# Kernel optimization log

Hardware: AMD Instinct MI355X
Metric: run time of the kernel (lower is better)

## Reference

```python
import jax, jax.numpy as jnp
import numpy as np

CH = 256
B, H, W = 8, 64, 64


def _conv1x1(x, w, b):
    # x: [b, cin, h, w], w: [cout, cin], b: [cout]
    return jnp.einsum('bchw,oc->bohw', x, w) + b[None, :, None, None]


def setup_inputs() -> dict:
    key = jax.random.key(0)
    ks = jax.random.split(key, 6)
    s = 0.05  # weight scale (spectral-norm keeps weights O(1); scaled for stable softmax)
    return {
        'x': jax.random.normal(ks[0], (B, CH, H, W), dtype=jnp.float32),
        'wf': jax.random.normal(ks[1], (CH // 8, CH), dtype=jnp.float32) * s,
        'bf': jnp.zeros((CH // 8,), dtype=jnp.float32),
        'wg': jax.random.normal(ks[2], (CH // 8, CH), dtype=jnp.float32) * s,
        'bg': jnp.zeros((CH // 8,), dtype=jnp.float32),
        'wh': jax.random.normal(ks[3], (CH // 2, CH), dtype=jnp.float32) * s,
        'bh': jnp.zeros((CH // 2,), dtype=jnp.float32),
        'wv': jax.random.normal(ks[4], (CH, CH // 2), dtype=jnp.float32) * s,
        'bv': jnp.zeros((CH,), dtype=jnp.float32),
        'gamma': jnp.ones((1,), dtype=jnp.float32) * 0.5,
    }


def reference(x, wf, bf, wg, bg, wh, bh, wv, bv, gamma):
    b, c, h, w = x.shape
    n = h * w
    f = _conv1x1(x, wf, bf).reshape(b, -1, n)   # [b, c/8, n]
    g = _conv1x1(x, wg, bg).reshape(b, -1, n)   # [b, c/8, n]
    # scores = f^T g : [b, n, n]; softmax over last dim
    beta = jax.nn.softmax(jnp.einsum('bkn,bkm->bnm', f, g), axis=-1)
    h_ = _conv1x1(x, wh, bh).reshape(b, -1, n)  # [b, c/2, n]
    o = jnp.einsum('bcn,bnm->bcm', h_, beta).reshape(b, c // 2, h, w)
    o = _conv1x1(o, wv, bv)                      # [b, c, h, w]
    return x + gamma[0] * o
```

## Files before the change

kernel.cpp:

```cpp
#include <hip/hip_runtime.h>
#include <cstdint>

typedef float f32x4 __attribute__((ext_vector_type(4)));
typedef short bf16x8 __attribute__((ext_vector_type(8)));
typedef unsigned short u16x4 __attribute__((ext_vector_type(4)));
typedef unsigned uint4v __attribute__((ext_vector_type(4)));
typedef unsigned uint2v __attribute__((ext_vector_type(2)));

#define LOG2E 1.44269504088896340736f

#if __has_builtin(__builtin_amdgcn_exp2f)
#define EXP2(v) __builtin_amdgcn_exp2f(v)
#else
#define EXP2(v) exp2f(v)
#endif
#if __has_builtin(__builtin_amdgcn_logf)
#define LOG2F(v) __builtin_amdgcn_logf(v)
#else
#define LOG2F(v) __log2f(v)
#endif

#define GLD16(gp, lp) __builtin_amdgcn_global_load_lds( \
    (const __attribute__((address_space(1))) unsigned*)(const void*)(gp), \
    (__attribute__((address_space(3))) unsigned*)(void*)(lp), 16, 0, 0)

enum : unsigned {
    WALL_OFF  = 0u,
    BALL_OFF  = 98304u,
    WVF_OFF   = 99072u,
    FF_OFF    = 164608u,
    GF_OFF    = 2261760u,
    HF_OFF    = 4358912u,
    SCALE_OFF = 12747520u,
    ZPART_OFF = 12878592u,
    PART_OFF  = 13402880u,
};

static __device__ __forceinline__ unsigned short f2bf(float f) {
    unsigned u = __builtin_bit_cast(unsigned, f);
    u += 0x7fffu + ((u >> 16) & 1u);
    return (unsigned short)(u >> 16);
}

static __device__ __forceinline__ unsigned pk_bf(float lo, float hi) {
    unsigned a = __builtin_bit_cast(unsigned, hi) + 0x8000u;
    unsigned b = __builtin_bit_cast(unsigned, lo) + 0x8000u;
    return __builtin_amdgcn_perm(a, b, 0x07060302u);
}

static __device__ __forceinline__ f32x4 mfma_bf16(bf16x8 a, bf16x8 b, f32x4 c) {
    return __builtin_amdgcn_mfma_f32_16x16x32_bf16(a, b, c, 0, 0, 0);
}

__global__ __launch_bounds__(256) void k0_pack(const float* __restrict__ wf,
                                               const float* __restrict__ bfv,
                                               const float* __restrict__ wg,
                                               const float* __restrict__ bg,
                                               const float* __restrict__ wh,
                                               const float* __restrict__ bh,
                                               const float* __restrict__ wv,
                                               unsigned char* __restrict__ ws) {
    unsigned idx = blockIdx.x * 256u + threadIdx.x;
    unsigned short* Wall = (unsigned short*)(ws + WALL_OFF);
    float* ball = (float*)(ws + BALL_OFF);
    unsigned short* wvf = (unsigned short*)(ws + WVF_OFF);
    if (idx < 49152u) {
        unsigned k = idx >> 8;
        float v;
        if (k < 32u)      v = wf[idx] * LOG2E;
        else if (k < 64u) v = wg[idx - 8192u];
        else              v = wh[idx - 16384u];
        Wall[idx] = f2bf(v);
    } else if (idx < 49344u) {
        unsigned k = idx - 49152u;
        float v;
        if (k < 32u)      v = bfv[k] * LOG2E;
        else if (k < 64u) v = bg[k - 32u];
        else              v = bh[k - 64u];
        ball[k] = v;
    } else if (idx < 82112u) {
        unsigned jj = idx - 49344u;
        unsigned cc = jj >> 7, c = jj & 127u;
        unsigned cct = cc >> 4, lv = cc & 15u;
        unsigned ksv = c >> 5, qv = (c >> 3) & 3u, jv = c & 7u;
        wvf[(((cct * 4u + ksv) * 4u + qv) * 16u + lv) * 8u + jv] = f2bf(wv[jj]);
    }
}

__global__ __launch_bounds__(256) void k1_proj(const float* __restrict__ x,
                                               unsigned char* __restrict__ ws) {
    __shared__ unsigned XT[64 * 132];
    const int b = blockIdx.y;
    const int n0 = blockIdx.x * 64;
    const unsigned short* Wall = (const unsigned short*)(ws + WALL_OFF);
    const float* ball = (const float*)(ws + BALL_OFF);
    unsigned short* Ff = (unsigned short*)(ws + FF_OFF) + b * 131072;
    unsigned short* Gf = (unsigned short*)(ws + GF_OFF) + b * 131072;
    unsigned short* Hf = (unsigned short*)(ws + HF_OFF) + b * 524288;
    const int tid = threadIdx.x;
    const float* xb = x + b * (256 * 4096) + n0;
    {
        const int n4 = (tid & 15) * 4;
        const int crow = (tid >> 4) * 2;
        #pragma unroll
        for (int it = 0; it < 8; ++it) {
            const int c = crow + it * 32;
            const f32x4 r0 = *(const f32x4*)&xb[(size_t)c * 4096 + n4];
            const f32x4 r1 = *(const f32x4*)&xb[(size_t)(c + 1) * 4096 + n4];
            #pragma unroll
            for (int j = 0; j < 4; ++j)
                XT[(n4 + j) * 132 + (c >> 1)] = pk_bf(r0[j], r1[j]);
        }
    }
    __syncthreads();
    const int l = tid & 15, q = (tid >> 4) & 3, w = tid >> 6;
    const int nloc = w * 16 + l;
    const int ncol = n0 + nloc;
    bf16x8 bX[8];
    #pragma unroll
    for (int ks = 0; ks < 8; ++ks)
        bX[ks] = *(const bf16x8*)&XT[nloc * 132 + ks * 16 + q * 4];
    #pragma unroll
    for (int kt = 0; kt < 12; ++kt) {
        f32x4 acc = {0.f, 0.f, 0.f, 0.f};
        #pragma unroll
        for (int ks = 0; ks < 8; ++ks) {
            bf16x8 aW = *(const bf16x8*)&Wall[(kt * 16 + l) * 256 + ks * 32 + q * 8];
            acc = mfma_bf16(aW, bX[ks], acc);
        }
        const int kr0 = kt * 16 + q * 4;
        #pragma unroll
        for (int r = 0; r < 4; ++r) acc[r] += ball[kr0 + r];
        if (kt < 4) {
            const int kk = kt & 1;
            unsigned short* dst = (kt < 2) ? Ff : Gf;
            const int nt = ncol >> 4;
            const int qf = kk * 2 + (q >> 1), j0 = (q & 1) * 4;
            u16x4 pk;
            #pragma unroll
            for (int r = 0; r < 4; ++r) pk[r] = f2bf(acc[r]);
            *(u16x4*)&dst[(nt * 64 + qf * 16 + l) * 8 + j0] = pk;
        } else {
            const int ct = kt - 4;
            const int nt = ncol >> 5, qh = (ncol >> 3) & 3, jh = ncol & 7;
            #pragma unroll
            for (int r = 0; r < 4; ++r)
                Hf[((nt * 8 + ct) * 64 + qh * 16 + (q * 4 + r)) * 8 + jh] = f2bf(acc[r]);
        }
    }
}

__global__ __launch_bounds__(256) void k2_stats(unsigned char* __restrict__ ws) {
    const int b = blockIdx.y, zsl = blockIdx.z, tid = threadIdx.x;
    const int lane = tid & 63, l = tid & 15, q = (tid >> 4) & 3, w = tid >> 6;
    const unsigned short* Ff = (const unsigned short*)(ws + FF_OFF) + b * 131072;
    const unsigned short* Gf = (const unsigned short*)(ws + GF_OFF) + b * 131072;
    float* Zp = (float*)(ws + ZPART_OFF) + zsl * 32768 + b * 4096;
    const int n0 = blockIdx.x * 256 + w * 64;
    const int nt0 = n0 >> 4;
    bf16x8 aF[4];
    #pragma unroll
    for (int t = 0; t < 4; ++t)
        aF[t] = *(const bf16x8*)&Ff[((nt0 + t) * 64 + lane) * 8];
    f32x4 z[4];
    #pragma unroll
    for (int t = 0; t < 4; ++t) z[t] = (f32x4){0.f, 0.f, 0.f, 0.f};
    const int mt0 = zsl * 64;
    bf16x8 bG = *(const bf16x8*)&Gf[(mt0 * 64 + lane) * 8];
    for (int mt = 0; mt < 64; ++mt) {
        const bf16x8 g = bG;
        if (mt + 1 < 64)
            bG = *(const bf16x8*)&Gf[((mt0 + mt + 1) * 64 + lane) * 8];
        #pragma unroll
        for (int t = 0; t < 4; ++t) {
            f32x4 s = mfma_bf16(aF[t], g, (f32x4){0.f, 0.f, 0.f, 0.f});
            #pragma unroll
            for (int r = 0; r < 4; ++r)
                z[t][r] += EXP2(s[r]);
        }
    }
    #pragma unroll
    for (int off = 1; off < 16; off <<= 1)
        #pragma unroll
        for (int t = 0; t < 4; ++t)
            #pragma unroll
            for (int r = 0; r < 4; ++r)
                z[t][r] += __shfl_xor(z[t][r], off, 64);
    if (l == 0) {
        #pragma unroll
        for (int t = 0; t < 4; ++t)
            #pragma unroll
            for (int r = 0; r < 4; ++r)
                Zp[n0 + t * 16 + q * 4 + r] = z[t][r];
    }
}

__global__ __launch_bounds__(256) void k2b_inv(unsigned char* __restrict__ ws) {
    const float* zp = (const float*)(ws + ZPART_OFF);
    float* scale = (float*)(ws + SCALE_OFF);
    const int idx = (blockIdx.x * 256 + threadIdx.x) * 4;
    f32x4 s = *(const f32x4*)&zp[idx];
    s += *(const f32x4*)&zp[32768 + idx];
    s += *(const f32x4*)&zp[65536 + idx];
    s += *(const f32x4*)&zp[98304 + idx];
    f32x4 o;
    #pragma unroll
    for (int r = 0; r < 4; ++r) o[r] = -LOG2F(s[r]);
    *(f32x4*)&scale[idx] = o;
}

template<int NS>
__global__ __launch_bounds__(256, NS) void k3_attn(unsigned char* __restrict__ ws) {
    constexpr int NITER = 128 / NS;
    constexpr int NGRP = 8 * NS;
    constexpr int NQ = 4096 / NS;
    __shared__ __align__(16) unsigned short HT[2][4096];
    __shared__ __align__(16) unsigned short FTs[2][1024];
    __shared__ __align__(16) float SC[NQ];
    const int tid = threadIdx.x;
    const int lane = tid & 63, l = tid & 15, q = (tid >> 4) & 3, w = tid >> 6;
    const int g = blockIdx.x % NGRP, bxm = blockIdx.x / NGRP;
    const int b = g / NS, nh = g % NS;
    const unsigned short* Ff = (const unsigned short*)(ws + FF_OFF) + b * 131072;
    const unsigned short* Gf = (const unsigned short*)(ws + GF_OFF) + b * 131072;
    const unsigned short* Hf = (const unsigned short*)(ws + HF_OFF) + b * 524288;
    const float* lsc = (const float*)(ws + SCALE_OFF) + b * 4096 + nh * NQ;
    const int mt0 = bxm * 8 + w * 2;
    const bf16x8 bG0 = *(const bf16x8*)&Gf[(mt0 * 64 + lane) * 8];
    const bf16x8 bG1 = *(const bf16x8*)&Gf[((mt0 + 1) * 64 + lane) * 8];
    f32x4 acc0[8], acc1[8];
    #pragma unroll
    for (int ct = 0; ct < 8; ++ct) {
        acc0[ct] = (f32x4){0.f, 0.f, 0.f, 0.f};
        acc1[ct] = (f32x4){0.f, 0.f, 0.f, 0.f};
    }
    const bool qlo = q < 2;
    const int srcA = (q & 1) * 32 + l;
    const int srcB = srcA + 16;

    auto stage = [&](int i, int p) {
        const unsigned short* Hg = Hf + (size_t)(nh * NITER + i) * 4096;
        GLD16(Hg + ((w * 2 + 0) * 64 + lane) * 8, &HT[p][(w * 2 + 0) * 512]);
        GLD16(Hg + ((w * 2 + 1) * 64 + lane) * 8, &HT[p][(w * 2 + 1) * 512]);
        if (w < 2)
            GLD16(Ff + ((size_t)((nh * NITER + i) * 2 + w) * 64 + lane) * 8,
                  &FTs[p][w * 512]);
    };

    {
        constexpr int CH = NQ / 256;
        #pragma unroll
        for (int j = w; j < CH; j += 4)
            GLD16(lsc + j * 256 + lane * 4, &SC[j * 256]);
    }
    stage(0, 0);

    for (int i = 0; i < NITER; ++i) {
        const int p = i & 1;
        __syncthreads();
        if (i + 1 < NITER) stage(i + 1, p ^ 1);
        const bf16x8 aF0 = *(const bf16x8*)&FTs[p][lane * 8];
        const bf16x8 aF1 = *(const bf16x8*)&FTs[p][512 + lane * 8];
        const f32x4 c0 = *(const f32x4*)&SC[i * 32 + q * 4];
        const f32x4 c1 = *(const f32x4*)&SC[i * 32 + 16 + q * 4];
        f32x4 s0 = mfma_bf16(aF0, bG0, c0);
        f32x4 s1 = mfma_bf16(aF1, bG0, c1);
        f32x4 s2 = mfma_bf16(aF0, bG1, c0);
        f32x4 s3 = mfma_bf16(aF1, bG1, c1);
        f32x4 e0, e1, e2, e3;
        #pragma unroll
        for (int r = 0; r < 4; ++r) {
            e0[r] = EXP2(s0[r]);
            e1[r] = EXP2(s1[r]);
            e2[r] = EXP2(s2[r]);
            e3[r] = EXP2(s3[r]);
        }
        const unsigned a01 = pk_bf(e0[0], e0[1]), a23 = pk_bf(e0[2], e0[3]);
        const unsigned b01 = pk_bf(e1[0], e1[1]), b23 = pk_bf(e1[2], e1[3]);
        const unsigned g01 = pk_bf(e2[0], e2[1]), g23 = pk_bf(e2[2], e2[3]);
        const unsigned h01 = pk_bf(e3[0], e3[1]), h23 = pk_bf(e3[2], e3[3]);
        uint4v r0, r1;
        {
            int tA, tB;
            tA = __shfl((int)a01, srcA, 64); tB = __shfl((int)b01, srcA, 64);
            r0[0] = (unsigned)(qlo ? tA : tB);
            tA = __shfl((int)a23, srcA, 64); tB = __shfl((int)b23, srcA, 64);
            r0[1] = (unsigned)(qlo ? tA : tB);
            tA = __shfl((int)a01, srcB, 64); tB = __shfl((int)b01, srcB, 64);
            r0[2] = (unsigned)(qlo ? tA : tB);
            tA = __shfl((int)a23, srcB, 64); tB = __shfl((int)b23, srcB, 64);
            r0[3] = (unsigned)(qlo ? tA : tB);
            tA = __shfl((int)g01, srcA, 64); tB = __shfl((int)h01, srcA, 64);
            r1[0] = (unsigned)(qlo ? tA : tB);
            tA = __shfl((int)g23, srcA, 64); tB = __shfl((int)h23, srcA, 64);
            r1[1] = (unsigned)(qlo ? tA : tB);
            tA = __shfl((int)g01, srcB, 64); tB = __shfl((int)h01, srcB, 64);
            r1[2] = (unsigned)(qlo ? tA : tB);
            tA = __shfl((int)g23, srcB, 64); tB = __shfl((int)h23, srcB, 64);
            r1[3] = (unsigned)(qlo ? tA : tB);
        }
        const bf16x8 bE0 = __builtin_bit_cast(bf16x8, r0);
        const bf16x8 bE1 = __builtin_bit_cast(bf16x8, r1);
        #pragma unroll
        for (int ct = 0; ct < 8; ++ct) {
            const bf16x8 aH = *(const bf16x8*)&HT[p][ct * 512 + lane * 8];
            acc0[ct] = mfma_bf16(aH, bE0, acc0[ct]);
            acc1[ct] = mfma_bf16(aH, bE1, acc1[ct]);
        }
    }
    unsigned short* P = (unsigned short*)(ws + PART_OFF);
    const size_t mb = (size_t)(b * NS + nh) * 4096 + bxm * 128;
    #pragma unroll
    for (int ct = 0; ct < 8; ++ct) {
        uint2v p0, p1;
        p0[0] = pk_bf(acc0[ct][0], acc0[ct][1]);
        p0[1] = pk_bf(acc0[ct][2], acc0[ct][3]);
        p1[0] = pk_bf(acc1[ct][0], acc1[ct][1]);
        p1[1] = pk_bf(acc1[ct][2], acc1[ct][3]);
        *(uint2v*)&P[(mb + w * 32 + l) * 128 + ct * 16 + q * 4] = p0;
        *(uint2v*)&P[(mb + w * 32 + 16 + l) * 128 + ct * 16 + q * 4] = p1;
    }
}

template<int NS>
__global__ __launch_bounds__(256) void k4_out(const float* __restrict__ x,
                                              const float* __restrict__ bv,
                                              const float* __restrict__ gamma,
                                              float* __restrict__ out,
                                              unsigned char* __restrict__ ws) {
    const int b = blockIdx.y, tid = threadIdx.x;
    const int lane = tid & 63, l = tid & 15, q = (tid >> 4) & 3, w = tid >> 6;
    const unsigned short* P = (const unsigned short*)(ws + PART_OFF);
    const unsigned short* Wvf = (const unsigned short*)(ws + WVF_OFF);
    const int mg = blockIdx.x * 64 + w * 16 + l;
    bf16x8 bO[4];
    #pragma unroll
    for (int ks = 0; ks < 4; ++ks) {
        float lo[4] = {0.f, 0.f, 0.f, 0.f}, hi[4] = {0.f, 0.f, 0.f, 0.f};
        #pragma unroll
        for (int h = 0; h < NS; ++h) {
            const size_t bh = ((size_t)(b * NS + h) * 4096 + mg) * 128;
            const uint4v u = *(const uint4v*)&P[bh + ks * 32 + q * 8];
            #pragma unroll
            for (int j = 0; j < 4; ++j) {
                lo[j] += __builtin_bit_cast(float, u[j] << 16);
                hi[j] += __builtin_bit_cast(float, u[j] & 0xffff0000u);
            }
        }
        uint4v s;
        #pragma unroll
        for (int j = 0; j < 4; ++j) s[j] = pk_bf(lo[j], hi[j]);
        bO[ks] = __builtin_bit_cast(bf16x8, s);
    }
    const float gam = gamma[0];
    const float* xb = x + b * (256 * 4096);
    float* ob = out + b * (256 * 4096);
    #pragma unroll
    for (int cct = 0; cct < 16; ++cct) {
        f32x4 f = {0.f, 0.f, 0.f, 0.f};
        #pragma unroll
        for (int ks = 0; ks < 4; ++ks) {
            const bf16x8 aV = *(const bf16x8*)&Wvf[((cct * 4 + ks) * 64 + lane) * 8];
            f = mfma_bf16(aV, bO[ks], f);
        }
        #pragma unroll
        for (int r = 0; r < 4; ++r) {
            const int cc = cct * 16 + q * 4 + r;
            ob[cc * 4096 + mg] = xb[cc * 4096 + mg] + gam * (f[r] + bv[cc]);
        }
    }
}

extern "C" void kernel_launch(void* const* d_in, const int* in_sizes, int n_in,
                              void* d_out, int out_size, void* d_ws, size_t ws_size,
                              hipStream_t stream) {
    const float* x   = (const float*)d_in[0];
    const float* wf  = (const float*)d_in[1];
    const float* bfv = (const float*)d_in[2];
    const float* wg  = (const float*)d_in[3];
    const float* bg  = (const float*)d_in[4];
    const float* wh  = (const float*)d_in[5];
    const float* bh  = (const float*)d_in[6];
    const float* wv  = (const float*)d_in[7];
    const float* bv  = (const float*)d_in[8];
    const float* gam = (const float*)d_in[9];
    float* out = (float*)d_out;
    unsigned char* ws = (unsigned char*)d_ws;
    (void)in_sizes; (void)n_in; (void)out_size;

    hipLaunchKernelGGL(k0_pack, dim3(321), dim3(256), 0, stream,
                       wf, bfv, wg, bg, wh, bh, wv, ws);
    hipLaunchKernelGGL(k1_proj, dim3(64, 8), dim3(256), 0, stream, x, ws);
    hipLaunchKernelGGL(k2_stats, dim3(16, 8, 4), dim3(256), 0, stream, ws);
    hipLaunchKernelGGL(k2b_inv, dim3(32), dim3(256), 0, stream, ws);

    const size_t need4 = (size_t)PART_OFF + (size_t)8 * 4 * 4096 * 128 * 2;
    if (ws_size >= need4) {
        hipLaunchKernelGGL(HIP_KERNEL_NAME(k3_attn<4>), dim3(1024), dim3(256),
                           0, stream, ws);
        hipLaunchKernelGGL(HIP_KERNEL_NAME(k4_out<4>), dim3(64, 8), dim3(256),
                           0, stream, x, bv, gam, out, ws);
    } else {
        hipLaunchKernelGGL(HIP_KERNEL_NAME(k3_attn<2>), dim3(512), dim3(256),
                           0, stream, ws);
        hipLaunchKernelGGL(HIP_KERNEL_NAME(k4_out<2>), dim3(64, 8), dim3(256),
                           0, stream, x, bv, gam, out, ws);
    }
}
```

Before: 219.1 us.

## Fuse softmax-normalizer and output projection into attention kernel via last-block counter

Removes the separate inverse-normalizer kernel by computing -log2 of the summed partial Z directly into shared memory at the start of the attention kernel. Also removes the separate output kernel: each attention block increments an atomic counter per (batch, m-tile), and the last of the NS split blocks reduces the partials and applies the Wv projection plus residual. This saves two launches and their tail gaps, but serializes the final reduction onto the last-arriving blocks. It also relies on the counters being zeroed in the pack kernel on every call.

Result: slower. 422.4 us (+92.8%).

```diff
diff --git a/kernel.cpp b/kernel.cpp
--- a/kernel.cpp
+++ b/kernel.cpp
@@ -31,9 +31,9 @@
     FF_OFF    = 164608u,
     GF_OFF    = 2261760u,
     HF_OFF    = 4358912u,
-    SCALE_OFF = 12747520u,
     ZPART_OFF = 12878592u,
-    PART_OFF  = 13402880u,
+    CTR_OFF   = 13402880u,
+    PART_OFF  = 13404928u,
 };
 
 static __device__ __forceinline__ unsigned short f2bf(float f) {
@@ -84,6 +84,8 @@
         unsigned cct = cc >> 4, lv = cc & 15u;
         unsigned ksv = c >> 5, qv = (c >> 3) & 3u, jv = c & 7u;
         wvf[(((cct * 4u + ksv) * 4u + qv) * 16u + lv) * 8u + jv] = f2bf(wv[jj]);
+    } else if (idx < 82624u) {
+        ((int*)(ws + CTR_OFF))[idx - 82112u] = 0;
     }
 }
 
@@ -195,28 +197,19 @@
     }
 }
 
-__global__ __launch_bounds__(256) void k2b_inv(unsigned char* __restrict__ ws) {
-    const float* zp = (const float*)(ws + ZPART_OFF);
-    float* scale = (float*)(ws + SCALE_OFF);
-    const int idx = (blockIdx.x * 256 + threadIdx.x) * 4;
-    f32x4 s = *(const f32x4*)&zp[idx];
-    s += *(const f32x4*)&zp[32768 + idx];
-    s += *(const f32x4*)&zp[65536 + idx];
-    s += *(const f32x4*)&zp[98304 + idx];
-    f32x4 o;
-    #pragma unroll
-    for (int r = 0; r < 4; ++r) o[r] = -LOG2F(s[r]);
-    *(f32x4*)&scale[idx] = o;
-}
-
 template<int NS>
-__global__ __launch_bounds__(256, NS) void k3_attn(unsigned char* __restrict__ ws) {
+__global__ __launch_bounds__(256, 4) void k3_attn(const float* __restrict__ x,
+                                                  const float* __restrict__ bv,
+                                                  const float* __restrict__ gamma,
+                                                  float* __restrict__ out,
+                                                  unsigned char* __restrict__ ws) {
     constexpr int NITER = 128 / NS;
     constexpr int NGRP = 8 * NS;
     constexpr int NQ = 4096 / NS;
     __shared__ __align__(16) unsigned short HT[2][4096];
     __shared__ __align__(16) unsigned short FTs[2][1024];
     __shared__ __align__(16) float SC[NQ];
+    __shared__ int lastFlag;
     const int tid = threadIdx.x;
     const int lane = tid & 63, l = tid & 15, q = (tid >> 4) & 3, w = tid >> 6;
     const int g = blockIdx.x % NGRP, bxm = blockIdx.x / NGRP;
@@ -224,7 +217,6 @@
     const unsigned short* Ff = (const unsigned short*)(ws + FF_OFF) + b * 131072;
     const unsigned short* Gf = (const unsigned short*)(ws + GF_OFF) + b * 131072;
     const unsigned short* Hf = (const unsigned short*)(ws + HF_OFF) + b * 524288;
-    const float* lsc = (const float*)(ws + SCALE_OFF) + b * 4096 + nh * NQ;
     const int mt0 = bxm * 8 + w * 2;
     const bf16x8 bG0 = *(const bf16x8*)&Gf[(mt0 * 64 + lane) * 8];
     const bf16x8 bG1 = *(const bf16x8*)&Gf[((mt0 + 1) * 64 + lane) * 8];
@@ -247,13 +239,15 @@
                   &FTs[p][w * 512]);
     };
 
+    stage(0, 0);
     {
-        constexpr int CH = NQ / 256;
-        #pragma unroll
-        for (int j = w; j < CH; j += 4)
-            GLD16(lsc + j * 256 + lane * 4, &SC[j * 256]);
-    }
-    stage(0, 0);
+        const float* zp = (const float*)(ws + ZPART_OFF) + b * 4096 + nh * NQ;
+        #pragma unroll
+        for (int j = tid; j < NQ; j += 256) {
+            const float s = zp[j] + zp[32768 + j] + zp[65536 + j] + zp[98304 + j];
+            SC[j] = -LOG2F(s);
+        }
+    }
 
     for (int i = 0; i < NITER; ++i) {
         const int p = i & 1;
@@ -320,53 +314,56 @@
         *(uint2v*)&P[(mb + w * 32 + l) * 128 + ct * 16 + q * 4] = p0;
         *(uint2v*)&P[(mb + w * 32 + 16 + l) * 128 + ct * 16 + q * 4] = p1;
     }
-}
-
-template<int NS>
-__global__ __launch_bounds__(256) void k4_out(const float* __restrict__ x,
-                                              const float* __restrict__ bv,
-                                              const float* __restrict__ gamma,
-                                              float* __restrict__ out,
-                                              unsigned char* __restrict__ ws) {
-    const int b = blockIdx.y, tid = threadIdx.x;
-    const int lane = tid & 63, l = tid & 15, q = (tid >> 4) & 3, w = tid >> 6;
-    const unsigned short* P = (const unsigned short*)(ws + PART_OFF);
+    __syncthreads();
+    if (tid == 0) {
+        __threadfence();
+        int* ctr = (int*)(ws + CTR_OFF);
+        const int old = atomicAdd(&ctr[b * 32 + bxm], 1);
+        lastFlag = (old == NS - 1) ? 1 : 0;
+    }
+    __syncthreads();
+    if (!lastFlag) return;
+    __threadfence();
+    const unsigned short* Pr = (const unsigned short*)(ws + PART_OFF);
     const unsigned short* Wvf = (const unsigned short*)(ws + WVF_OFF);
-    const int mg = blockIdx.x * 64 + w * 16 + l;
-    bf16x8 bO[4];
-    #pragma unroll
-    for (int ks = 0; ks < 4; ++ks) {
-        float lo[4] = {0.f, 0.f, 0.f, 0.f}, hi[4] = {0.f, 0.f, 0.f, 0.f};
-        #pragma unroll
-        for (int h = 0; h < NS; ++h) {
-            const size_t bh = ((size_t)(b * NS + h) * 4096 + mg) * 128;
-            const uint4v u = *(const uint4v*)&P[bh + ks * 32 + q * 8];
-            #pragma unroll
-            for (int j = 0; j < 4; ++j) {
-                lo[j] += __builtin_bit_cast(float, u[j] << 16);
-                hi[j] += __builtin_bit_cast(float, u[j] & 0xffff0000u);
-            }
-        }
-        uint4v s;
-        #pragma unroll
-        for (int j = 0; j < 4; ++j) s[j] = pk_bf(lo[j], hi[j]);
-        bO[ks] = __builtin_bit_cast(bf16x8, s);
-    }
     const float gam = gamma[0];
     const float* xb = x + b * (256 * 4096);
     float* ob = out + b * (256 * 4096);
     #pragma unroll
-    for (int cct = 0; cct < 16; ++cct) {
-        f32x4 f = {0.f, 0.f, 0.f, 0.f};
+    for (int msub = 0; msub < 2; ++msub) {
+        const int mg = bxm * 128 + msub * 64 + w * 16 + l;
+        bf16x8 bO[4];
         #pragma unroll
         for (int ks = 0; ks < 4; ++ks) {
-            const bf16x8 aV = *(const bf16x8*)&Wvf[((cct * 4 + ks) * 64 + lane) * 8];
-            f = mfma_bf16(aV, bO[ks], f);
-        }
-        #pragma unroll
-        for (int r = 0; r < 4; ++r) {
-            const int cc = cct * 16 + q * 4 + r;
-            ob[cc * 4096 + mg] = xb[cc * 4096 + mg] + gam * (f[r] + bv[cc]);
+            float lo[4] = {0.f, 0.f, 0.f, 0.f}, hi[4] = {0.f, 0.f, 0.f, 0.f};
+            #pragma unroll
+            for (int h = 0; h < NS; ++h) {
+                const size_t bh = ((size_t)(b * NS + h) * 4096 + mg) * 128;
+                const uint4v u = *(const uint4v*)&Pr[bh + ks * 32 + q * 8];
+                #pragma unroll
+                for (int j = 0; j < 4; ++j) {
+                    lo[j] += __builtin_bit_cast(float, u[j] << 16);
+                    hi[j] += __builtin_bit_cast(float, u[j] & 0xffff0000u);
+                }
+            }
+            uint4v s;
+            #pragma unroll
+            for (int j = 0; j < 4; ++j) s[j] = pk_bf(lo[j], hi[j]);
+            bO[ks] = __builtin_bit_cast(bf16x8, s);
+        }
+        #pragma unroll
+        for (int cct = 0; cct < 16; ++cct) {
+            f32x4 f = {0.f, 0.f, 0.f, 0.f};
+            #pragma unroll
+            for (int ks = 0; ks < 4; ++ks) {
+                const bf16x8 aV = *(const bf16x8*)&Wvf[((cct * 4 + ks) * 64 + lane) * 8];
+                f = mfma_bf16(aV, bO[ks], f);
+            }
+            #pragma unroll
+            for (int r = 0; r < 4; ++r) {
+                const int cc = cct * 16 + q * 4 + r;
+                ob[cc * 4096 + mg] = xb[cc * 4096 + mg] + gam * (f[r] + bv[cc]);
+            }
         }
     }
 }
@@ -388,22 +385,17 @@
     unsigned char* ws = (unsigned char*)d_ws;
     (void)in_sizes; (void)n_in; (void)out_size;
 
-    hipLaunchKernelGGL(k0_pack, dim3(321), dim3(256), 0, stream,
+    hipLaunchKernelGGL(k0_pack, dim3(322), dim3(256), 0, stream,
                        wf, bfv, wg, bg, wh, bh, wv, ws);
     hipLaunchKernelGGL(k1_proj, dim3(64, 8), dim3(256), 0, stream, x, ws);
     hipLaunchKernelGGL(k2_stats, dim3(16, 8, 4), dim3(256), 0, stream, ws);
-    hipLaunchKernelGGL(k2b_inv, dim3(32), dim3(256), 0, stream, ws);
 
     const size_t need4 = (size_t)PART_OFF + (size_t)8 * 4 * 4096 * 128 * 2;
     if (ws_size >= need4) {
         hipLaunchKernelGGL(HIP_KERNEL_NAME(k3_attn<4>), dim3(1024), dim3(256),
-                           0, stream, ws);
-        hipLaunchKernelGGL(HIP_KERNEL_NAME(k4_out<4>), dim3(64, 8), dim3(256),
                            0, stream, x, bv, gam, out, ws);
     } else {
         hipLaunchKernelGGL(HIP_KERNEL_NAME(k3_attn<2>), dim3(512), dim3(256),
-                           0, stream, ws);
-        hipLaunchKernelGGL(HIP_KERNEL_NAME(k4_out<2>), dim3(64, 8), dim3(256),
                            0, stream, x, bv, gam, out, ws);
     }
 }
```

## Fuse softmax-normalizer kernel into attention and add eight-way key split

Applied to the files above, without the earlier changes.

Removes the separate k2b_inv launch and computes the per-query log-sum normalizer directly inside k3_attn from the four partial Z sums. It also adds an NS=8 split of the key dimension (2048 blocks) when the workspace is large enough, and fixes launch bounds at 4 waves per SIMD. This saves one kernel launch and a global round trip for the scale, and raises parallelism in the attention stage. In exchange, the k4 reduction must combine more partials and the normalizer work is repeated in every block.

After: 247.9 us. 13.2% more time.

```diff
diff --git a/kernel.cpp b/kernel.cpp
--- a/kernel.cpp
+++ b/kernel.cpp
@@ -31,9 +31,8 @@
     FF_OFF    = 164608u,
     GF_OFF    = 2261760u,
     HF_OFF    = 4358912u,
-    SCALE_OFF = 12747520u,
     ZPART_OFF = 12878592u,
-    PART_OFF  = 13402880u,
+    PART_OFF  = 13404928u,
 };
 
 static __device__ __forceinline__ unsigned short f2bf(float f) {
@@ -195,22 +194,8 @@
     }
 }
 
-__global__ __launch_bounds__(256) void k2b_inv(unsigned char* __restrict__ ws) {
-    const float* zp = (const float*)(ws + ZPART_OFF);
-    float* scale = (float*)(ws + SCALE_OFF);
-    const int idx = (blockIdx.x * 256 + threadIdx.x) * 4;
-    f32x4 s = *(const f32x4*)&zp[idx];
-    s += *(const f32x4*)&zp[32768 + idx];
-    s += *(const f32x4*)&zp[65536 + idx];
-    s += *(const f32x4*)&zp[98304 + idx];
-    f32x4 o;
-    #pragma unroll
-    for (int r = 0; r < 4; ++r) o[r] = -LOG2F(s[r]);
-    *(f32x4*)&scale[idx] = o;
-}
-
 template<int NS>
-__global__ __launch_bounds__(256, NS) void k3_attn(unsigned char* __restrict__ ws) {
+__global__ __launch_bounds__(256, 4) void k3_attn(unsigned char* __restrict__ ws) {
     constexpr int NITER = 128 / NS;
     constexpr int NGRP = 8 * NS;
     constexpr int NQ = 4096 / NS;
@@ -224,7 +209,6 @@
     const unsigned short* Ff = (const unsigned short*)(ws + FF_OFF) + b * 131072;
     const unsigned short* Gf = (const unsigned short*)(ws + GF_OFF) + b * 131072;
     const unsigned short* Hf = (const unsigned short*)(ws + HF_OFF) + b * 524288;
-    const float* lsc = (const float*)(ws + SCALE_OFF) + b * 4096 + nh * NQ;
     const int mt0 = bxm * 8 + w * 2;
     const bf16x8 bG0 = *(const bf16x8*)&Gf[(mt0 * 64 + lane) * 8];
     const bf16x8 bG1 = *(const bf16x8*)&Gf[((mt0 + 1) * 64 + lane) * 8];
@@ -247,13 +231,15 @@
                   &FTs[p][w * 512]);
     };
 
+    stage(0, 0);
     {
-        constexpr int CH = NQ / 256;
-        #pragma unroll
-        for (int j = w; j < CH; j += 4)
-            GLD16(lsc + j * 256 + lane * 4, &SC[j * 256]);
-    }
-    stage(0, 0);
+        const float* zp = (const float*)(ws + ZPART_OFF) + b * 4096 + nh * NQ;
+        #pragma unroll
+        for (int j = tid; j < NQ; j += 256) {
+            const float s = zp[j] + zp[32768 + j] + zp[65536 + j] + zp[98304 + j];
+            SC[j] = -LOG2F(s);
+        }
+    }
 
     for (int i = 0; i < NITER; ++i) {
         const int p = i & 1;
@@ -392,10 +378,15 @@
                        wf, bfv, wg, bg, wh, bh, wv, ws);
     hipLaunchKernelGGL(k1_proj, dim3(64, 8), dim3(256), 0, stream, x, ws);
     hipLaunchKernelGGL(k2_stats, dim3(16, 8, 4), dim3(256), 0, stream, ws);
-    hipLaunchKernelGGL(k2b_inv, dim3(32), dim3(256), 0, stream, ws);
-
-    const size_t need4 = (size_t)PART_OFF + (size_t)8 * 4 * 4096 * 128 * 2;
-    if (ws_size >= need4) {
+
+    const size_t base = (size_t)PART_OFF;
+    const size_t per  = (size_t)8 * 4096 * 128 * 2;
+    if (ws_size >= base + 8 * per) {
+        hipLaunchKernelGGL(HIP_KERNEL_NAME(k3_attn<8>), dim3(2048), dim3(256),
+                           0, stream, ws);
+        hipLaunchKernelGGL(HIP_KERNEL_NAME(k4_out<8>), dim3(64, 8), dim3(256),
+                           0, stream, x, bv, gam, out, ws);
+    } else if (ws_size >= base + 4 * per) {
         hipLaunchKernelGGL(HIP_KERNEL_NAME(k3_attn<4>), dim3(1024), dim3(256),
                            0, stream, ws);
         hipLaunchKernelGGL(HIP_KERNEL_NAME(k4_out<4>), dim3(64, 8), dim3(256),
```
